# Kernel tuning notes

Measured on AMD Instinct MI355X. Metric: run time of the kernel, lower is better.

## Reference

```python
import jax, jax.numpy as jnp
import numpy as np
from jax import lax

B, T, D, U, SIG = 256, 1024, 256, 128, 20

def setup_inputs() -> dict:
    key = jax.random.key(0)
    ks = jax.random.split(key, 6)
    return {
        "inputs": jax.random.normal(ks[0], (B, T, D), dtype=jnp.float32),
        "signatures": jax.random.normal(ks[1], (B, T, SIG), dtype=jnp.float32),
        "input_kernel": jax.random.normal(ks[2], (D, 3 * U), dtype=jnp.float32) * 0.05,
        "recurrent_kernel": jax.random.normal(ks[3], (U, 3 * U), dtype=jnp.float32) * 0.05,
        "forget_kernel": jax.random.normal(ks[4], (SIG, U), dtype=jnp.float32) * 0.05,
        "bias": jnp.zeros((4 * U,), dtype=jnp.float32),
    }

def reference(inputs, signatures, input_kernel, recurrent_kernel, forget_kernel, bias):
    # inputs: [B,T,D], signatures: [B,T,SIG]
    b, t, d = inputs.shape
    u = recurrent_kernel.shape[0]
    b_i, b_f, b_c, b_o = jnp.split(bias, 4, axis=-1)
    h0 = jnp.zeros((b, u), dtype=inputs.dtype)
    c0 = jnp.zeros((b, u), dtype=inputs.dtype)
    # precompute the time-parallel projections (same math as per-step)
    x_proj = jnp.einsum('btd,du->btu', inputs, input_kernel)            # [B,T,3U]
    f_seq = jax.nn.sigmoid(jnp.einsum('bts,su->btu', signatures, forget_kernel) + b_f)  # [B,T,U]

    def step(carry, xs):
        x_t, f_t = xs                     # [B,3U], [B,U]
        h_prev, c_prev = carry
        gates = jnp.dot(h_prev, recurrent_kernel) + x_t
        i_t, c_hat, o_t = jnp.split(gates, 3, axis=-1)
        i_t = jax.nn.sigmoid(i_t + b_i)
        c_hat = jnp.tanh(c_hat + b_c)
        o_t = jax.nn.sigmoid(o_t + b_o)
        c_new = f_t * c_prev + i_t * c_hat
        h_new = o_t * jnp.tanh(c_new)
        return (h_new, c_new), h_new

    scan_xs = (x_proj.transpose(1, 0, 2), f_seq.transpose(1, 0, 2))    # time-major
    (_, _), h_seq = lax.scan(step, (h0, c0), scan_xs)
    return h_seq.transpose(1, 0, 2)                                    # [B,T,U]
```

## Files before the change

### kernel.cpp

```cpp
#include <hip/hip_runtime.h>

typedef _Float16 f16;
typedef _Float16 f16x2 __attribute__((ext_vector_type(2)));
typedef _Float16 f16x4 __attribute__((ext_vector_type(4)));
typedef _Float16 f16x8 __attribute__((ext_vector_type(8)));
typedef float f32x4 __attribute__((ext_vector_type(4)));

#define NB 256
#define NT 1024
#define ND 256
#define NU 128
#define NSIG 20
#define N3U 384
#define BT (NB * NT)
#define CH 16
#define NCHUNK (NT / CH)

#define BM 128
#define BN 128
#define BK 32
#define LDK 40

static __device__ __forceinline__ float sigmoid_fast(float x) {
    return __builtin_amdgcn_rcpf(1.f + __expf(-x));
}
static __device__ __forceinline__ float tanh_fast(float x) {
    return 1.f - 2.f * __builtin_amdgcn_rcpf(__expf(2.f * x) + 1.f);
}

__global__ __launch_bounds__(256) void xproj_gemm(
    const float* __restrict__ A,
    const float* __restrict__ Wk,
    f16* __restrict__ out)
{
    const int n0 = blockIdx.x * BN;
    const int m0 = blockIdx.y * BM;
    const int tid = threadIdx.x;
    const int lane = tid & 63;
    const int w = tid >> 6;
    const int mm = lane & 15;
    const int q = lane >> 4;
    const int wr = w >> 1;
    const int wc = w & 1;

    __shared__ __align__(16) f16 sA[BM * LDK];
    __shared__ __align__(16) f16 sB[BN * LDK];

    f32x4 acc[4][4];
    #pragma unroll
    for (int i = 0; i < 4; ++i)
        #pragma unroll
        for (int j = 0; j < 4; ++j)
            acc[i][j] = (f32x4){0.f, 0.f, 0.f, 0.f};

    const int ar = tid >> 1;
    const int ac = (tid & 1) * 16;
    const int bn = tid >> 1;
    const int bk = (tid & 1) * 16;

    for (int kt = 0; kt < ND; kt += BK) {
        const float* ap = A + (size_t)(m0 + ar) * ND + kt + ac;
        const float4 a0 = *(const float4*)(ap + 0);
        const float4 a1 = *(const float4*)(ap + 4);
        const float4 a2 = *(const float4*)(ap + 8);
        const float4 a3 = *(const float4*)(ap + 12);

        f16x8 bv0, bv1;
        #pragma unroll
        for (int i = 0; i < 8; ++i)
            bv0[i] = (f16)Wk[(size_t)(kt + bk + i) * N3U + n0 + bn];
        #pragma unroll
        for (int i = 0; i < 8; ++i)
            bv1[i] = (f16)Wk[(size_t)(kt + bk + 8 + i) * N3U + n0 + bn];

        f16x8 av0, av1;
        av0[0]=(f16)a0.x; av0[1]=(f16)a0.y; av0[2]=(f16)a0.z; av0[3]=(f16)a0.w;
        av0[4]=(f16)a1.x; av0[5]=(f16)a1.y; av0[6]=(f16)a1.z; av0[7]=(f16)a1.w;
        av1[0]=(f16)a2.x; av1[1]=(f16)a2.y; av1[2]=(f16)a2.z; av1[3]=(f16)a2.w;
        av1[4]=(f16)a3.x; av1[5]=(f16)a3.y; av1[6]=(f16)a3.z; av1[7]=(f16)a3.w;

        *(f16x8*)(sA + ar * LDK + ac)     = av0;
        *(f16x8*)(sA + ar * LDK + ac + 8) = av1;
        *(f16x8*)(sB + bn * LDK + bk)     = bv0;
        *(f16x8*)(sB + bn * LDK + bk + 8) = bv1;

        __syncthreads();

        f16x8 afrag[4], bfrag[4];
        #pragma unroll
        for (int mi = 0; mi < 4; ++mi)
            afrag[mi] = *(const f16x8*)(sA + (wr * 64 + mi * 16 + mm) * LDK + q * 8);
        #pragma unroll
        for (int ni = 0; ni < 4; ++ni)
            bfrag[ni] = *(const f16x8*)(sB + (wc * 64 + ni * 16 + mm) * LDK + q * 8);

        #pragma unroll
        for (int mi = 0; mi < 4; ++mi)
            #pragma unroll
            for (int ni = 0; ni < 4; ++ni)
                acc[mi][ni] = __builtin_amdgcn_mfma_f32_16x16x32_f16(
                    afrag[mi], bfrag[ni], acc[mi][ni], 0, 0, 0);

        __syncthreads();
    }

    #pragma unroll
    for (int mi = 0; mi < 4; ++mi) {
        #pragma unroll
        for (int ni = 0; ni < 4; ++ni) {
            #pragma unroll
            for (int r = 0; r < 4; ++r) {
                const int row = m0 + wr * 64 + mi * 16 + q * 4 + r;
                const int col = n0 + wc * 64 + ni * 16 + mm;
                out[(size_t)row * N3U + col] = (f16)acc[mi][ni][r];
            }
        }
    }
}

__global__ __launch_bounds__(256) void fgate_kernel(
    const float* __restrict__ sig,
    const float* __restrict__ Wf,
    const float* __restrict__ bias,
    f16* __restrict__ fout)
{
    __shared__ float sWf[NSIG * NU];
    __shared__ float sSig[8 * NSIG];
    const int tid = threadIdx.x;
    const int bt0 = blockIdx.x * 8;

    for (int i = tid; i < NSIG * NU; i += 256)
        sWf[i] = Wf[i];
    if (tid < 8 * NSIG)
        sSig[tid] = sig[(size_t)bt0 * NSIG + tid];
    __syncthreads();

    const int r = tid >> 5;
    const int u0 = (tid & 31) * 4;

    float a0 = bias[NU + u0 + 0];
    float a1 = bias[NU + u0 + 1];
    float a2 = bias[NU + u0 + 2];
    float a3 = bias[NU + u0 + 3];
    #pragma unroll
    for (int s = 0; s < NSIG; ++s) {
        const float sv = sSig[r * NSIG + s];
        const float4 wv = *(const float4*)(&sWf[s * NU + u0]);
        a0 += sv * wv.x; a1 += sv * wv.y; a2 += sv * wv.z; a3 += sv * wv.w;
    }
    f16x4 o;
    o[0] = (f16)sigmoid_fast(a0);
    o[1] = (f16)sigmoid_fast(a1);
    o[2] = (f16)sigmoid_fast(a2);
    o[3] = (f16)sigmoid_fast(a3);
    *(f16x4*)(&fout[(size_t)(bt0 + r) * NU + u0]) = o;
}

__global__ __launch_bounds__(384, 2) void recur_kernel(
    const f16* __restrict__ xp,
    const f16* __restrict__ fg,
    const float* __restrict__ Wr,
    const float* __restrict__ bias,
    float* __restrict__ out)
{
    const int b = blockIdx.x;
    const int j = threadIdx.x;

    __shared__ __align__(16) f16 x_sh[2][CH * N3U];
    __shared__ __align__(16) f16 f_sh[2][CH * NU];
    __shared__ __align__(16) float o_sh[CH * NU];
    __shared__ __align__(16) f16 h_sh[2][NU];
    __shared__ __align__(16) float gate_sh[N3U];

    f16x2 wr[64];
    #pragma unroll
    for (int k2 = 0; k2 < 64; ++k2) {
        const float w0 = Wr[(size_t)(2 * k2) * N3U + j];
        const float w1 = Wr[(size_t)(2 * k2 + 1) * N3U + j];
        f16x2 p; p[0] = (f16)w0; p[1] = (f16)w1;
        wr[k2] = p;
    }

    float bi = 0.f, bc = 0.f, bo = 0.f, cstate = 0.f;
    if (j < NU) {
        bi = bias[j];
        bc = bias[2 * NU + j];
        bo = bias[3 * NU + j];
        h_sh[0][j] = (f16)0.f;
    }

    {
        const uint4* xsrc = (const uint4*)(xp + ((size_t)b * NT) * N3U);
        uint4* xdst = (uint4*)x_sh[0];
        xdst[j] = xsrc[j];
        xdst[j + 384] = xsrc[j + 384];
        if (j < 256) {
            const uint4* fsrc = (const uint4*)(fg + ((size_t)b * NT) * NU);
            ((uint4*)f_sh[0])[j] = fsrc[j];
        }
    }
    __syncthreads();

    int p = 0;
    for (int c = 0; c < NCHUNK; ++c) {
        const int bb = c & 1;

        uint4 xs0, xs1, fs0;
        const bool have_next = (c + 1 < NCHUNK);
        if (have_next) {
            const uint4* xsrc = (const uint4*)(xp + ((size_t)b * NT + (size_t)(c + 1) * CH) * N3U);
            xs0 = xsrc[j];
            xs1 = xsrc[j + 384];
            if (j < 256) {
                const uint4* fsrc = (const uint4*)(fg + ((size_t)b * NT + (size_t)(c + 1) * CH) * NU);
                fs0 = fsrc[j];
            }
        }

        for (int t = 0; t < CH; ++t) {
            float g0 = (float)x_sh[bb][t * N3U + j], g1 = 0.f, g2 = 0.f, g3 = 0.f;
            const uint4* h4 = (const uint4*)h_sh[p];
            #pragma unroll
            for (int kk = 0; kk < 16; ++kk) {
                const uint4 hv = h4[kk];
                g0 = __builtin_amdgcn_fdot2(__builtin_bit_cast(f16x2, hv.x), wr[kk * 4 + 0], g0, false);
                g1 = __builtin_amdgcn_fdot2(__builtin_bit_cast(f16x2, hv.y), wr[kk * 4 + 1], g1, false);
                g2 = __builtin_amdgcn_fdot2(__builtin_bit_cast(f16x2, hv.z), wr[kk * 4 + 2], g2, false);
                g3 = __builtin_amdgcn_fdot2(__builtin_bit_cast(f16x2, hv.w), wr[kk * 4 + 3], g3, false);
            }
            gate_sh[j] = (g0 + g1) + (g2 + g3);
            __syncthreads();

            if (j < NU) {
                const float gi = gate_sh[j] + bi;
                const float gc = gate_sh[j + NU] + bc;
                const float go = gate_sh[j + 2 * NU] + bo;
                const float it = sigmoid_fast(gi);
                const float chv = tanh_fast(gc);
                const float ot = sigmoid_fast(go);
                const float ft = (float)f_sh[bb][t * NU + j];
                cstate = ft * cstate + it * chv;
                const float h = ot * tanh_fast(cstate);
                o_sh[t * NU + j] = h;
                h_sh[p ^ 1][j] = (f16)h;
            }
            __syncthreads();
            p ^= 1;
        }

        {
            uint4* dst = (uint4*)(out + ((size_t)b * NT + (size_t)c * CH) * NU);
            const uint4* src = (const uint4*)o_sh;
            if (j < 256) {
                dst[j] = src[j];
                dst[j + 256] = src[j + 256];
            }
        }

        if (have_next) {
            uint4* xdst = (uint4*)x_sh[bb ^ 1];
            xdst[j] = xs0;
            xdst[j + 384] = xs1;
            if (j < 256) ((uint4*)f_sh[bb ^ 1])[j] = fs0;
        }
        __syncthreads();
    }
}

extern "C" void kernel_launch(void* const* d_in, const int* in_sizes, int n_in,
                              void* d_out, int out_size, void* d_ws, size_t ws_size,
                              hipStream_t stream) {
    const float* inputs = (const float*)d_in[0];
    const float* sig    = (const float*)d_in[1];
    const float* Wk     = (const float*)d_in[2];
    const float* Wr     = (const float*)d_in[3];
    const float* Wf     = (const float*)d_in[4];
    const float* bias   = (const float*)d_in[5];
    float* out = (float*)d_out;

    f16* xp = (f16*)d_ws;
    f16* fg = (f16*)((char*)d_ws + (size_t)BT * N3U * sizeof(f16));

    xproj_gemm<<<dim3(N3U / BN, BT / BM), 256, 0, stream>>>(inputs, Wk, xp);
    fgate_kernel<<<dim3(BT / 8), 256, 0, stream>>>(sig, Wf, bias, fg);
    recur_kernel<<<dim3(NB), 384, 0, stream>>>(xp, fg, Wr, bias, out);

    (void)in_sizes; (void)n_in; (void)out_size; (void)ws_size;
}
```

Before: 1.198 ms.

## Batch four sequences per block and compute recurrent matmul with MFMA

The recurrent kernel now handles four batch rows per block with 512 threads. The h·Wr product for all rows goes through 16x16x32 f16 MFMA instructions, with Wr held in registers as MFMA B-fragments, instead of per-thread fdot2 loops over a single row. The chunked shared-memory staging of x/f is replaced by a two-step register prefetch, and outputs are written straight to global memory each step. This cuts the serial per-step latency per sequence and raises arithmetic density. The trade-offs are 64 blocks instead of 256 (lower occupancy across CUs) and 12 of the 16 MFMA rows doing wasted work on zero padding.

```diff
diff --git a/kernel.cpp b/kernel.cpp
--- a/kernel.cpp
+++ b/kernel.cpp
@@ -13,13 +13,14 @@
 #define NSIG 20
 #define N3U 384
 #define BT (NB * NT)
-#define CH 16
-#define NCHUNK (NT / CH)
 
 #define BM 128
 #define BN 128
 #define BK 32
 #define LDK 40
+
+#define RB 4
+#define RTHREADS 512
 
 static __device__ __forceinline__ float sigmoid_fast(float x) {
     return __builtin_amdgcn_rcpf(1.f + __expf(-x));
@@ -156,112 +157,105 @@
     *(f16x4*)(&fout[(size_t)(bt0 + r) * NU + u0]) = o;
 }
 
-__global__ __launch_bounds__(384, 2) void recur_kernel(
+__global__ __launch_bounds__(RTHREADS, 2) void recur_kernel(
     const f16* __restrict__ xp,
     const f16* __restrict__ fg,
     const float* __restrict__ Wr,
     const float* __restrict__ bias,
     float* __restrict__ out)
 {
-    const int b = blockIdx.x;
-    const int j = threadIdx.x;
-
-    __shared__ __align__(16) f16 x_sh[2][CH * N3U];
-    __shared__ __align__(16) f16 f_sh[2][CH * NU];
-    __shared__ __align__(16) float o_sh[CH * NU];
-    __shared__ __align__(16) f16 h_sh[2][NU];
-    __shared__ __align__(16) float gate_sh[N3U];
-
-    f16x2 wr[64];
-    #pragma unroll
-    for (int k2 = 0; k2 < 64; ++k2) {
-        const float w0 = Wr[(size_t)(2 * k2) * N3U + j];
-        const float w1 = Wr[(size_t)(2 * k2 + 1) * N3U + j];
-        f16x2 p; p[0] = (f16)w0; p[1] = (f16)w1;
-        wr[k2] = p;
-    }
-
-    float bi = 0.f, bc = 0.f, bo = 0.f, cstate = 0.f;
-    if (j < NU) {
-        bi = bias[j];
-        bc = bias[2 * NU + j];
-        bo = bias[3 * NU + j];
-        h_sh[0][j] = (f16)0.f;
-    }
-
-    {
-        const uint4* xsrc = (const uint4*)(xp + ((size_t)b * NT) * N3U);
-        uint4* xdst = (uint4*)x_sh[0];
-        xdst[j] = xsrc[j];
-        xdst[j + 384] = xsrc[j + 384];
-        if (j < 256) {
-            const uint4* fsrc = (const uint4*)(fg + ((size_t)b * NT) * NU);
-            ((uint4*)f_sh[0])[j] = fsrc[j];
-        }
-    }
+    const int tid = threadIdx.x;
+    const int lane = tid & 63;
+    const int w = tid >> 6;
+    const int ml = lane & 15;
+    const int kg = lane >> 4;
+    const int b0 = blockIdx.x * RB;
+
+    const int ab = tid >> 7;
+    const int au = tid & 127;
+
+    __shared__ __align__(16) f16 H[16 * 136];
+    __shared__ __align__(16) float G[4 * 388];
+
+    for (int i = tid; i < 16 * 136; i += RTHREADS) H[i] = (f16)0.f;
+
+    f16x8 wrv[3][4];
+    #pragma unroll
+    for (int j = 0; j < 3; ++j) {
+        const int n = w * 48 + j * 16 + ml;
+        #pragma unroll
+        for (int kt = 0; kt < 4; ++kt) {
+            #pragma unroll
+            for (int i = 0; i < 8; ++i) {
+                const int k = kt * 32 + kg * 8 + i;
+                wrv[j][kt][i] = (f16)Wr[(size_t)k * N3U + n];
+            }
+        }
+    }
+
+    const float bi = bias[au];
+    const float bc = bias[2 * NU + au];
+    const float bo = bias[3 * NU + au];
+    float cst = 0.f;
+
+    f16 xi[2], xc[2], xo[2], ffr[2];
+    const size_t xrow0 = ((size_t)(b0 + ab) * NT) * N3U + au;
+    const size_t frow0 = ((size_t)(b0 + ab) * NT) * NU + au;
+    #pragma unroll
+    for (int s = 0; s < 2; ++s) {
+        xi[s]  = xp[xrow0 + (size_t)s * N3U];
+        xc[s]  = xp[xrow0 + (size_t)s * N3U + NU];
+        xo[s]  = xp[xrow0 + (size_t)s * N3U + 2 * NU];
+        ffr[s] = fg[frow0 + (size_t)s * NU];
+    }
+
     __syncthreads();
 
-    int p = 0;
-    for (int c = 0; c < NCHUNK; ++c) {
-        const int bb = c & 1;
-
-        uint4 xs0, xs1, fs0;
-        const bool have_next = (c + 1 < NCHUNK);
-        if (have_next) {
-            const uint4* xsrc = (const uint4*)(xp + ((size_t)b * NT + (size_t)(c + 1) * CH) * N3U);
-            xs0 = xsrc[j];
-            xs1 = xsrc[j + 384];
-            if (j < 256) {
-                const uint4* fsrc = (const uint4*)(fg + ((size_t)b * NT + (size_t)(c + 1) * CH) * NU);
-                fs0 = fsrc[j];
+    const int hbase = ml * 136 + kg * 8;
+    for (int t = 0; t < NT; ++t) {
+        f16x8 af[4];
+        #pragma unroll
+        for (int kt = 0; kt < 4; ++kt)
+            af[kt] = *(const f16x8*)(H + hbase + kt * 32);
+
+        f32x4 acc[3];
+        #pragma unroll
+        for (int j = 0; j < 3; ++j) acc[j] = (f32x4){0.f, 0.f, 0.f, 0.f};
+        #pragma unroll
+        for (int kt = 0; kt < 4; ++kt)
+            #pragma unroll
+            for (int j = 0; j < 3; ++j)
+                acc[j] = __builtin_amdgcn_mfma_f32_16x16x32_f16(
+                    af[kt], wrv[j][kt], acc[j], 0, 0, 0);
+
+        if (kg == 0) {
+            #pragma unroll
+            for (int j = 0; j < 3; ++j) {
+                const int col = w * 48 + j * 16 + ml;
+                #pragma unroll
+                for (int r = 0; r < 4; ++r)
+                    G[r * 388 + col] = acc[j][r];
             }
         }
-
-        for (int t = 0; t < CH; ++t) {
-            float g0 = (float)x_sh[bb][t * N3U + j], g1 = 0.f, g2 = 0.f, g3 = 0.f;
-            const uint4* h4 = (const uint4*)h_sh[p];
-            #pragma unroll
-            for (int kk = 0; kk < 16; ++kk) {
-                const uint4 hv = h4[kk];
-                g0 = __builtin_amdgcn_fdot2(__builtin_bit_cast(f16x2, hv.x), wr[kk * 4 + 0], g0, false);
-                g1 = __builtin_amdgcn_fdot2(__builtin_bit_cast(f16x2, hv.y), wr[kk * 4 + 1], g1, false);
-                g2 = __builtin_amdgcn_fdot2(__builtin_bit_cast(f16x2, hv.z), wr[kk * 4 + 2], g2, false);
-                g3 = __builtin_amdgcn_fdot2(__builtin_bit_cast(f16x2, hv.w), wr[kk * 4 + 3], g3, false);
-            }
-            gate_sh[j] = (g0 + g1) + (g2 + g3);
-            __syncthreads();
-
-            if (j < NU) {
-                const float gi = gate_sh[j] + bi;
-                const float gc = gate_sh[j + NU] + bc;
-                const float go = gate_sh[j + 2 * NU] + bo;
-                const float it = sigmoid_fast(gi);
-                const float chv = tanh_fast(gc);
-                const float ot = sigmoid_fast(go);
-                const float ft = (float)f_sh[bb][t * NU + j];
-                cstate = ft * cstate + it * chv;
-                const float h = ot * tanh_fast(cstate);
-                o_sh[t * NU + j] = h;
-                h_sh[p ^ 1][j] = (f16)h;
-            }
-            __syncthreads();
-            p ^= 1;
-        }
-
-        {
-            uint4* dst = (uint4*)(out + ((size_t)b * NT + (size_t)c * CH) * NU);
-            const uint4* src = (const uint4*)o_sh;
-            if (j < 256) {
-                dst[j] = src[j];
-                dst[j + 256] = src[j + 256];
-            }
-        }
-
-        if (have_next) {
-            uint4* xdst = (uint4*)x_sh[bb ^ 1];
-            xdst[j] = xs0;
-            xdst[j + 384] = xs1;
-            if (j < 256) ((uint4*)f_sh[bb ^ 1])[j] = fs0;
+        __syncthreads();
+
+        const int s = t & 1;
+        const float gi = G[ab * 388 + au]          + (float)xi[s]  + bi;
+        const float gc = G[ab * 388 + NU + au]     + (float)xc[s]  + bc;
+        const float go = G[ab * 388 + 2 * NU + au] + (float)xo[s]  + bo;
+        const float it = sigmoid_fast(gi);
+        const float ch = tanh_fast(gc);
+        const float ot = sigmoid_fast(go);
+        cst = (float)ffr[s] * cst + it * ch;
+        const float h = ot * tanh_fast(cst);
+        H[ab * 136 + au] = (f16)h;
+        out[((size_t)(b0 + ab) * NT + t) * NU + au] = h;
+
+        if (t + 2 < NT) {
+            xi[s]  = xp[xrow0 + (size_t)(t + 2) * N3U];
+            xc[s]  = xp[xrow0 + (size_t)(t + 2) * N3U + NU];
+            xo[s]  = xp[xrow0 + (size_t)(t + 2) * N3U + 2 * NU];
+            ffr[s] = fg[frow0 + (size_t)(t + 2) * NU];
         }
         __syncthreads();
     }
@@ -283,7 +277,7 @@
 
     xproj_gemm<<<dim3(N3U / BN, BT / BM), 256, 0, stream>>>(inputs, Wk, xp);
     fgate_kernel<<<dim3(BT / 8), 256, 0, stream>>>(sig, Wf, bias, fg);
-    recur_kernel<<<dim3(NB), 384, 0, stream>>>(xp, fg, Wr, bias, out);
+    recur_kernel<<<dim3(NB / RB), RTHREADS, 0, stream>>>(xp, fg, Wr, bias, out);
 
     (void)in_sizes; (void)n_in; (void)out_size; (void)ws_size;
 }
```

Result: slower. 1.759 ms (+46.8%).
